# Kernel tuning notes

Measured on AMD Instinct MI355X. Metric: run time of the kernel, lower is better.

## Reference

```python
import jax, jax.numpy as jnp
import numpy as np

T, H, W = 4, 16, 16
S = T * H * W          # 1024 flattened sequence length
C = 576                # embd_dim
NH = 8                 # n_head
DK = C // NH           # 72 per-head dim
L = 4                  # n_layer
B = 4                  # batch
PD = C // 3            # 192 per-axis pos-embed dim


def setup_inputs() -> dict:
    key = jax.random.key(0)
    ks = jax.random.split(key, 10)
    s = 1.0 / np.sqrt(C)
    return {
        "x": jax.random.normal(ks[0], (B, T, H, W, C), jnp.float32),
        "pos0": jax.random.normal(ks[1], (T, PD), jnp.float32) * 0.01,
        "pos1": jax.random.normal(ks[2], (H, PD), jnp.float32) * 0.01,
        "pos2": jax.random.normal(ks[3], (W, PD), jnp.float32) * 0.01,
        "ln1_g": jnp.ones((L, C), jnp.float32),
        "ln1_b": jnp.zeros((L, C), jnp.float32),
        "wq": jax.random.normal(ks[4], (L, C, C), jnp.float32) * s,
        "wk": jax.random.normal(ks[5], (L, C, C), jnp.float32) * s,
        "wv": jax.random.normal(ks[6], (L, C, C), jnp.float32) * s,
        "wo": jax.random.normal(ks[7], (L, C, C), jnp.float32) * (s / np.sqrt(L)),
        "wo_b": jnp.zeros((L, C), jnp.float32),
        "ln2_g": jnp.ones((L, C), jnp.float32),
        "ln2_b": jnp.zeros((L, C), jnp.float32),
        "w1": jax.random.normal(ks[8], (L, C, 4 * C), jnp.float32) * s,
        "b1": jnp.zeros((L, 4 * C), jnp.float32),
        "w2": jax.random.normal(ks[9], (L, 4 * C, C), jnp.float32) * (s / 2.0),
        "b2": jnp.zeros((L, C), jnp.float32),
    }


def _layernorm(x, g, b):
    # Faithful to the source: float32 math, and (1e-5 + rsqrt(var)) multiplier
    # (note: source adds eps to rsqrt, not to var -- replicated exactly).
    xf = x.astype(jnp.float32)
    mu = xf.mean(-1, keepdims=True)
    var = jnp.mean(jnp.square(xf - mu), -1, keepdims=True)
    y = (xf - mu) * (1e-5 + jax.lax.rsqrt(var)) * g + b
    return y.astype(x.dtype)


def _stack(x, pos0, pos1, pos2, ln1_g, ln1_b, wq, wk, wv, wo, wo_b,
           ln2_g, ln2_b, w1, b1, w2, b2):
    b = x.shape[0]
    xf = x.reshape(b, S, C)
    # right_shift (decode_step=None): shift flattened tokens right by one
    xf = jnp.pad(xf[:, :-1], ((0, 0), (1, 0), (0, 0)))
    # broadcast positional embedding, concat along channel
    pos = jnp.concatenate([
        jnp.broadcast_to(pos0[:, None, None, :], (T, H, W, PD)),
        jnp.broadcast_to(pos1[None, :, None, :], (T, H, W, PD)),
        jnp.broadcast_to(pos2[None, None, :, :], (T, H, W, PD)),
    ], axis=-1).reshape(S, C)
    xf = xf + pos

    causal = jnp.tril(jnp.ones((S, S), bool))
    scale = 1.0 / np.sqrt(DK)
    neg_inf = jnp.float32(-jnp.inf)

    for l in range(L):  # fixed small layer loop
        # --- causal full self-attention ---
        h = _layernorm(xf, ln1_g[l], ln1_b[l])
        q = (h @ wq[l]).reshape(b, S, NH, DK).transpose(0, 2, 1, 3)
        k = (h @ wk[l]).reshape(b, S, NH, DK).transpose(0, 2, 1, 3)
        v = (h @ wv[l]).reshape(b, S, NH, DK).transpose(0, 2, 1, 3)
        att = jnp.einsum('bhqd,bhkd->bhqk', q, k) * scale
        att = jnp.where(causal, att, neg_inf)
        att = jax.nn.softmax(att, axis=-1)
        a = jnp.einsum('bhqk,bhkd->bhqd', att, v)
        a = a.transpose(0, 2, 1, 3).reshape(b, S, C)
        xf = xf + a @ wo[l] + wo_b[l]
        # --- FFN with GeLU2: sigmoid(1.702*x)*x ---
        h = _layernorm(xf, ln2_g[l], ln2_b[l])
        h = h @ w1[l] + b1[l]
        h = jax.nn.sigmoid(1.702 * h) * h
        xf = xf + h @ w2[l] + b2[l]
    return xf.reshape(b, T, H, W, C)


def reference(x, pos0, pos1, pos2, ln1_g, ln1_b, wq, wk, wv, wo, wo_b,
              ln2_g, ln2_b, w1, b1, w2, b2):
    return _stack(x, pos0, pos1, pos2, ln1_g, ln1_b, wq, wk, wv, wo, wo_b,
                  ln2_g, ln2_b, w1, b1, w2, b2)
```

## Files before the change

### kernel.cpp

```cpp
#include <hip/hip_runtime.h>
#include <hip/hip_bf16.h>

typedef __hip_bfloat16 bf16;
using bf16x8 = __attribute__((ext_vector_type(8))) short;
using f32x4  = __attribute__((ext_vector_type(4))) float;

#define S_LEN 1024
#define CDIM  576
#define NHEAD 8
#define DKH   72
#define BATCH 4
#define MROWS 4096
#define FFDIM 2304
#define QKVN  1728

__device__ __forceinline__ void gload16(const void* g, void* l) {
  __builtin_amdgcn_global_load_lds(
      (const __attribute__((address_space(1))) unsigned int*)g,
      (__attribute__((address_space(3))) unsigned int*)l, 16, 0, 0);
}

__device__ __forceinline__ short f2bf_bits(float x) {
  unsigned int u = __float_as_uint(x);
  u += 0x7fffu + ((u >> 16) & 1u);
  return (short)(u >> 16);
}

__global__ __launch_bounds__(256) void transpose_cvt(
    const float* __restrict__ in, bf16* __restrict__ out, int K, int N,
    size_t in_ls, size_t out_ls) {
  __shared__ float tile[32][33];
  const float* inl = in + (size_t)blockIdx.z * in_ls;
  bf16* outl = out + (size_t)blockIdx.z * out_ls;
  int n0 = blockIdx.x * 32, k0 = blockIdx.y * 32;
  int tx = threadIdx.x & 31, ty = threadIdx.x >> 5;
#pragma unroll
  for (int i = 0; i < 32; i += 8)
    tile[ty + i][tx] = inl[(size_t)(k0 + ty + i) * N + (n0 + tx)];
  __syncthreads();
#pragma unroll
  for (int i = 0; i < 32; i += 8)
    outl[(size_t)(n0 + ty + i) * K + (k0 + tx)] = __float2bfloat16(tile[tx][ty + i]);
}

__global__ __launch_bounds__(256) void build_xf(
    const float* __restrict__ x, const float* __restrict__ p0,
    const float* __restrict__ p1, const float* __restrict__ p2,
    float* __restrict__ xf) {
  int idx = blockIdx.x * 256 + threadIdx.x;
  int c4 = idx % 144;
  int s  = (idx / 144) & (S_LEN - 1);
  int b  = idx / (144 * S_LEN);
  int c  = c4 * 4;
  int t = s >> 8, hh = (s >> 4) & 15, w = s & 15;
  float4 pv;
  if (c < 192)       pv = *(const float4*)&p0[t  * 192 + c];
  else if (c < 384)  pv = *(const float4*)&p1[hh * 192 + c - 192];
  else               pv = *(const float4*)&p2[w  * 192 + c - 384];
  float4 xv = make_float4(0.f, 0.f, 0.f, 0.f);
  if (s > 0) xv = *(const float4*)&x[((size_t)b * S_LEN + s - 1) * CDIM + c];
  float4 r = make_float4(xv.x + pv.x, xv.y + pv.y, xv.z + pv.z, xv.w + pv.w);
  *(float4*)&xf[((size_t)b * S_LEN + s) * CDIM + c] = r;
}

__global__ __launch_bounds__(256) void ln_kernel(
    const float* __restrict__ x, const float* __restrict__ g,
    const float* __restrict__ b, bf16* __restrict__ out) {
  int row  = blockIdx.x * 4 + (threadIdx.x >> 6);
  int lane = threadIdx.x & 63;
  const float* xr = x + (size_t)row * CDIM;
  float vals[9];
  float sum = 0.f;
#pragma unroll
  for (int i = 0; i < 9; i++) { vals[i] = xr[lane + 64 * i]; sum += vals[i]; }
#pragma unroll
  for (int o = 1; o < 64; o <<= 1) sum += __shfl_xor(sum, o);
  float mu = sum * (1.f / CDIM);
  float vs = 0.f;
#pragma unroll
  for (int i = 0; i < 9; i++) { float d = vals[i] - mu; vs += d * d; }
#pragma unroll
  for (int o = 1; o < 64; o <<= 1) vs += __shfl_xor(vs, o);
  float mult = 1e-5f + rsqrtf(vs * (1.f / CDIM));
  bf16* orow = out + (size_t)row * CDIM;
#pragma unroll
  for (int i = 0; i < 9; i++) {
    int c = lane + 64 * i;
    orow[c] = __float2bfloat16((vals[i] - mu) * mult * g[c] + b[c]);
  }
}

template <int BM, int BN, bool BIAS, bool RES, int ACT, bool OUTBF>
__global__ __launch_bounds__(256) void gemm3(
    const bf16* __restrict__ A, const bf16* __restrict__ Bt,
    const float* __restrict__ bias, const float* __restrict__ res,
    void* __restrict__ outp, int N, int K) {
  constexpr int MI = BM / 32;
  constexpr int NI = BN / 32;
  constexpr int AJ = BM / 64;
  constexpr int BJ = BN / 64;
  __shared__ __align__(16) short ldsA[2][BM * 32];
  __shared__ __align__(16) short ldsB[2][BN * 32];
  const int tid = threadIdx.x, lane = tid & 63, wave = tid >> 6;
  const int lr = lane & 15, quad = lane >> 4;
  const int m0 = blockIdx.x * BM, n0 = blockIdx.y * BN;
  const int wm = (wave & 1) * (BM / 2), wn = (wave >> 1) * (BN / 2);
  f32x4 acc[MI][NI] = {};

  const int srow = lane >> 2, scol = (lane & 3) * 8;
  const short* Ag[AJ];
  int ldsAo[AJ];
#pragma unroll
  for (int j = 0; j < AJ; j++) {
    Ag[j] = (const short*)A + (size_t)(m0 + (wave * AJ + j) * 16 + srow) * K + scol;
    ldsAo[j] = (wave * AJ + j) * 512;
  }
  const short* Bg[BJ];
  int ldsBo[BJ];
#pragma unroll
  for (int j = 0; j < BJ; j++) {
    Bg[j] = (const short*)Bt + (size_t)(n0 + (wave * BJ + j) * 16 + srow) * K + scol;
    ldsBo[j] = (wave * BJ + j) * 512;
  }

#pragma unroll
  for (int j = 0; j < AJ; j++) gload16(Ag[j], &ldsA[0][ldsAo[j]]);
#pragma unroll
  for (int j = 0; j < BJ; j++) gload16(Bg[j], &ldsB[0][ldsBo[j]]);
  __syncthreads();

  int cur = 0;
  for (int k0 = 0; k0 < K; k0 += 32) {
    const int nxt = cur ^ 1;
    if (k0 + 32 < K) {
#pragma unroll
      for (int j = 0; j < AJ; j++) gload16(Ag[j] + k0 + 32, &ldsA[nxt][ldsAo[j]]);
#pragma unroll
      for (int j = 0; j < BJ; j++) gload16(Bg[j] + k0 + 32, &ldsB[nxt][ldsBo[j]]);
    }
    bf16x8 af[MI], bfv[NI];
#pragma unroll
    for (int mi = 0; mi < MI; mi++)
      af[mi] = *(const bf16x8*)&ldsA[cur][(wm + mi * 16 + lr) * 32 + quad * 8];
#pragma unroll
    for (int ni = 0; ni < NI; ni++)
      bfv[ni] = *(const bf16x8*)&ldsB[cur][(wn + ni * 16 + lr) * 32 + quad * 8];
#pragma unroll
    for (int mi = 0; mi < MI; mi++)
#pragma unroll
      for (int ni = 0; ni < NI; ni++)
        acc[mi][ni] = __builtin_amdgcn_mfma_f32_16x16x32_bf16(af[mi], bfv[ni], acc[mi][ni], 0, 0, 0);
    if (k0 + 32 < K) __syncthreads();
    cur = nxt;
  }

  float* fout = (float*)outp;
  bf16*  bout = (bf16*)outp;
#pragma unroll
  for (int mi = 0; mi < MI; mi++)
#pragma unroll
    for (int ni = 0; ni < NI; ni++) {
      int col = n0 + wn + ni * 16 + lr;
#pragma unroll
      for (int r = 0; r < 4; r++) {
        int row = m0 + wm + mi * 16 + quad * 4 + r;
        float v = acc[mi][ni][r];
        if (BIAS) v += bias[col];
        if (ACT == 1) v = v / (1.f + __expf(-1.702f * v));
        size_t idx = (size_t)row * N + col;
        if (RES) v += res[idx];
        if (OUTBF) bout[idx] = __float2bfloat16(v);
        else       fout[idx] = v;
      }
    }
}

__global__ __launch_bounds__(256) void attn_mfma(
    const bf16* __restrict__ qkv, bf16* __restrict__ a) {
  __shared__ __align__(16) short ldsK[2][9 * 512];
  __shared__ __align__(16) short ldsVt[2][80][104];
  __shared__ __align__(16) short ldsP[4 * 1024];
  const int bh = blockIdx.y, b = bh >> 3, h = bh & 7;
  const int tid = threadIdx.x, wave = tid >> 6, lane = tid & 63;
  const int lr = lane & 15, quad = lane >> 4;
  const int qt = 15 - (int)blockIdx.x;
  const float scale = 0.11785113019775793f;
  const int qcol = h * DKH, kcol = CDIM + h * DKH, vcol = 2 * CDIM + h * DKH;

  const int qrow = qt * 64 + wave * 16 + lr;
  const short* qg = (const short*)qkv + (size_t)(b * S_LEN + qrow) * QKVN + qcol;
  bf16x8 qfrag[3];
#pragma unroll
  for (int c = 0; c < 3; c++) {
    int d0 = c * 32 + quad * 8;
    bf16x8 z = {0, 0, 0, 0, 0, 0, 0, 0};
    qfrag[c] = (d0 < DKH) ? *(const bf16x8*)(qg + d0) : z;
  }
  f32x4 oacc[5] = {};
  float m[4], l[4];
#pragma unroll
  for (int r = 0; r < 4; r++) { m[r] = -1e30f; l[r] = 0.f; }

  const size_t ktstep = (size_t)64 * QKVN;
  const short* kg0 = (const short*)qkv + (size_t)(b * S_LEN + wave * 16 + lr) * QKVN + kcol + quad * 8;
  const short* kg2 = (const short*)qkv + (size_t)(b * S_LEN + lane) * QKVN + kcol + 64;
  const int vkey = tid & 63, vdgb = tid >> 6;
  const short* vg0 = (const short*)qkv + (size_t)(b * S_LEN + vkey) * QKVN + vcol;

  {
#pragma unroll
    for (int c = 0; c < 2; c++)
      gload16(kg0 + c * 32, &ldsK[0][(wave * 2 + c) * 512]);
    if (wave == 0) gload16(kg2, &ldsK[0][8 * 512]);
#pragma unroll
    for (int pass = 0; pass < 3; pass++) {
      int d0 = (vdgb + pass * 4) * 8;
      if (d0 < 80) {
        bf16x8 vv = {0, 0, 0, 0, 0, 0, 0, 0};
        if (d0 < DKH) vv = *(const bf16x8*)(vg0 + d0);
#pragma unroll
        for (int j = 0; j < 8; j++) ldsVt[0][d0 + j][vkey] = vv[j];
      }
    }
  }
  __syncthreads();

  for (int kt = 0; kt <= qt; kt++) {
    const int cur = kt & 1, nxt = cur ^ 1;
    const bool pf = (kt < qt);
    bf16x8 vpre[3];
    if (pf) {
      const short* kg = kg0 + (size_t)(kt + 1) * ktstep;
#pragma unroll
      for (int c = 0; c < 2; c++)
        gload16(kg + c * 32, &ldsK[nxt][(wave * 2 + c) * 512]);
      if (wave == 0) gload16(kg2 + (size_t)(kt + 1) * ktstep, &ldsK[nxt][8 * 512]);
      const short* vg = vg0 + (size_t)(kt + 1) * ktstep;
#pragma unroll
      for (int pass = 0; pass < 3; pass++) {
        int d0 = (vdgb + pass * 4) * 8;
        bf16x8 z = {0, 0, 0, 0, 0, 0, 0, 0};
        vpre[pass] = (d0 < DKH) ? *(const bf16x8*)(vg + d0) : z;
      }
    }
    f32x4 sacc[4] = {};
#pragma unroll
    for (int nc = 0; nc < 4; nc++) {
      bf16x8 kf0 = *(const bf16x8*)&ldsK[cur][(nc * 2 + 0) * 512 + lane * 8];
      sacc[nc] = __builtin_amdgcn_mfma_f32_16x16x32_bf16(qfrag[0], kf0, sacc[nc], 0, 0, 0);
      bf16x8 kf1 = *(const bf16x8*)&ldsK[cur][(nc * 2 + 1) * 512 + lane * 8];
      sacc[nc] = __builtin_amdgcn_mfma_f32_16x16x32_bf16(qfrag[1], kf1, sacc[nc], 0, 0, 0);
      bf16x8 kf2 = *(const bf16x8*)&ldsK[cur][8 * 512 + (nc * 16 + lr) * 8];
      sacc[nc] = __builtin_amdgcn_mfma_f32_16x16x32_bf16(qfrag[2], kf2, sacc[nc], 0, 0, 0);
    }
    float tmax[4];
#pragma unroll
    for (int r = 0; r < 4; r++) tmax[r] = -1e30f;
    bool diag = (kt == qt);
#pragma unroll
    for (int nc = 0; nc < 4; nc++)
#pragma unroll
      for (int r = 0; r < 4; r++) {
        float s = sacc[nc][r] * scale;
        if (diag && (nc * 16 + lr > wave * 16 + quad * 4 + r)) s = -1e30f;
        sacc[nc][r] = s;
        tmax[r] = fmaxf(tmax[r], s);
      }
#pragma unroll
    for (int r = 0; r < 4; r++) {
      tmax[r] = fmaxf(tmax[r], __shfl_xor(tmax[r], 1));
      tmax[r] = fmaxf(tmax[r], __shfl_xor(tmax[r], 2));
      tmax[r] = fmaxf(tmax[r], __shfl_xor(tmax[r], 4));
      tmax[r] = fmaxf(tmax[r], __shfl_xor(tmax[r], 8));
    }
    float alpha[4], psum[4];
#pragma unroll
    for (int r = 0; r < 4; r++) {
      float mn = fmaxf(m[r], tmax[r]);
      alpha[r] = __expf(m[r] - mn);
      m[r] = mn;
      psum[r] = 0.f;
    }
#pragma unroll
    for (int nc = 0; nc < 4; nc++)
#pragma unroll
      for (int r = 0; r < 4; r++) {
        float p = __expf(sacc[nc][r] - m[r]);
        psum[r] += p;
        int col = nc * 16 + lr;
        ldsP[wave * 1024 + (col >> 5) * 512 +
             (((col >> 3) & 3) * 16 + quad * 4 + r) * 8 + (col & 7)] = f2bf_bits(p);
      }
#pragma unroll
    for (int r = 0; r < 4; r++) {
      psum[r] += __shfl_xor(psum[r], 1);
      psum[r] += __shfl_xor(psum[r], 2);
      psum[r] += __shfl_xor(psum[r], 4);
      psum[r] += __shfl_xor(psum[r], 8);
      l[r] = l[r] * alpha[r] + psum[r];
    }
#pragma unroll
    for (int dc = 0; dc < 5; dc++)
#pragma unroll
      for (int r = 0; r < 4; r++) oacc[dc][r] *= alpha[r];
    __builtin_amdgcn_sched_barrier(0);
    bf16x8 pfrag[2];
#pragma unroll
    for (int kc = 0; kc < 2; kc++)
      pfrag[kc] = *(const bf16x8*)&ldsP[wave * 1024 + kc * 512 + lane * 8];
#pragma unroll
    for (int dc = 0; dc < 5; dc++)
#pragma unroll
      for (int kc = 0; kc < 2; kc++) {
        bf16x8 vf = *(const bf16x8*)&ldsVt[cur][dc * 16 + lr][kc * 32 + quad * 8];
        oacc[dc] = __builtin_amdgcn_mfma_f32_16x16x32_bf16(pfrag[kc], vf, oacc[dc], 0, 0, 0);
      }
    if (pf) {
#pragma unroll
      for (int pass = 0; pass < 3; pass++) {
        int d0 = (vdgb + pass * 4) * 8;
        if (d0 < 80) {
#pragma unroll
          for (int j = 0; j < 8; j++) ldsVt[nxt][d0 + j][vkey] = vpre[pass][j];
        }
      }
    }
    __syncthreads();
  }

#pragma unroll
  for (int dc = 0; dc < 5; dc++) {
    int d = dc * 16 + lr;
    if (d < DKH) {
#pragma unroll
      for (int r = 0; r < 4; r++) {
        int row = qt * 64 + wave * 16 + quad * 4 + r;
        float val = oacc[dc][r] / l[r];
        a[(size_t)(b * S_LEN + row) * CDIM + h * DKH + d] = __float2bfloat16(val);
      }
    }
  }
}

extern "C" void kernel_launch(void* const* d_in, const int* in_sizes, int n_in,
                              void* d_out, int out_size, void* d_ws, size_t ws_size,
                              hipStream_t stream) {
  const float* x    = (const float*)d_in[0];
  const float* pos0 = (const float*)d_in[1];
  const float* pos1 = (const float*)d_in[2];
  const float* pos2 = (const float*)d_in[3];
  const float* ln1g = (const float*)d_in[4];
  const float* ln1b = (const float*)d_in[5];
  const float* wq   = (const float*)d_in[6];
  const float* wk   = (const float*)d_in[7];
  const float* wv   = (const float*)d_in[8];
  const float* wo   = (const float*)d_in[9];
  const float* wob  = (const float*)d_in[10];
  const float* ln2g = (const float*)d_in[11];
  const float* ln2b = (const float*)d_in[12];
  const float* w1   = (const float*)d_in[13];
  const float* b1   = (const float*)d_in[14];
  const float* w2   = (const float*)d_in[15];
  const float* b2   = (const float*)d_in[16];

  char* ws = (char*)d_ws;
  size_t off = 0;
  auto alloc = [&](size_t bytes) {
    char* p = ws + off;
    off += (bytes + 255) & ~(size_t)255;
    return p;
  };
  bf16* wqkvT = (bf16*)alloc((size_t)4 * QKVN * CDIM * sizeof(bf16));
  bf16* woT   = (bf16*)alloc((size_t)4 * CDIM * CDIM * sizeof(bf16));
  bf16* w1T   = (bf16*)alloc((size_t)4 * FFDIM * CDIM * sizeof(bf16));
  bf16* w2T   = (bf16*)alloc((size_t)4 * CDIM * FFDIM * sizeof(bf16));
  bf16* hbuf  = (bf16*)alloc((size_t)MROWS * CDIM * sizeof(bf16));
  bf16* abuf  = (bf16*)alloc((size_t)MROWS * CDIM * sizeof(bf16));
  bf16* ubuf  = (bf16*)alloc((size_t)MROWS * FFDIM * sizeof(bf16));
  bf16* qkvb  = (bf16*)alloc((size_t)MROWS * QKVN * sizeof(bf16));
  float* xf   = (float*)d_out;

  const size_t ils  = (size_t)CDIM * CDIM;
  const size_t ils2 = (size_t)CDIM * FFDIM;
  const size_t qkv_ls = (size_t)QKVN * CDIM;
  transpose_cvt<<<dim3(18, 18, 4), 256, 0, stream>>>(wq, wqkvT, CDIM, CDIM, ils, qkv_ls);
  transpose_cvt<<<dim3(18, 18, 4), 256, 0, stream>>>(wk, wqkvT + (size_t)CDIM * CDIM, CDIM, CDIM, ils, qkv_ls);
  transpose_cvt<<<dim3(18, 18, 4), 256, 0, stream>>>(wv, wqkvT + (size_t)2 * CDIM * CDIM, CDIM, CDIM, ils, qkv_ls);
  transpose_cvt<<<dim3(18, 18, 4), 256, 0, stream>>>(wo, woT, CDIM, CDIM, ils, ils);
  transpose_cvt<<<dim3(72, 18, 4), 256, 0, stream>>>(w1, w1T, CDIM, FFDIM, ils2, ils2);
  transpose_cvt<<<dim3(18, 72, 4), 256, 0, stream>>>(w2, w2T, FFDIM, CDIM, ils2, ils2);

  build_xf<<<2304, 256, 0, stream>>>(x, pos0, pos1, pos2, xf);

  for (int l = 0; l < 4; l++) {
    bf16* wqkv_l = wqkvT + (size_t)l * qkv_ls;
    bf16* wo_l   = woT   + (size_t)l * ils;
    bf16* w1_l   = w1T   + (size_t)l * ils2;
    bf16* w2_l   = w2T   + (size_t)l * ils2;

    ln_kernel<<<1024, 256, 0, stream>>>(xf, ln1g + l * CDIM, ln1b + l * CDIM, hbuf);
    gemm3<128, 64, false, false, 0, true><<<dim3(32, QKVN / 64), 256, 0, stream>>>(
        hbuf, wqkv_l, nullptr, nullptr, qkvb, QKVN, CDIM);
    attn_mfma<<<dim3(16, 32), 256, 0, stream>>>(qkvb, abuf);
    gemm3<64, 64, true, true, 0, false><<<dim3(64, CDIM / 64), 256, 0, stream>>>(
        abuf, wo_l, wob + l * CDIM, xf, xf, CDIM, CDIM);
    ln_kernel<<<1024, 256, 0, stream>>>(xf, ln2g + l * CDIM, ln2b + l * CDIM, hbuf);
    gemm3<128, 64, true, false, 1, true><<<dim3(32, FFDIM / 64), 256, 0, stream>>>(
        hbuf, w1_l, b1 + l * FFDIM, nullptr, ubuf, FFDIM, CDIM);
    gemm3<64, 64, true, true, 0, false><<<dim3(64, CDIM / 64), 256, 0, stream>>>(
        ubuf, w2_l, b2 + l * CDIM, xf, xf, CDIM, FFDIM);
  }
}
```

Measured before the change: 779.7 us.

## Deepen GEMM LDS pipeline to four stages with prefetch distance two

```diff
diff --git a/kernel.cpp b/kernel.cpp
--- a/kernel.cpp
+++ b/kernel.cpp
@@ -18,6 +18,14 @@
   __builtin_amdgcn_global_load_lds(
       (const __attribute__((address_space(1))) unsigned int*)g,
       (__attribute__((address_space(3))) unsigned int*)l, 16, 0, 0);
+}
+
+template <int N> __device__ __forceinline__ void wait_vmcnt() {
+  if constexpr (N == 0)      asm volatile("s_waitcnt vmcnt(0)" ::: "memory");
+  else if constexpr (N == 2) asm volatile("s_waitcnt vmcnt(2)" ::: "memory");
+  else if constexpr (N == 3) asm volatile("s_waitcnt vmcnt(3)" ::: "memory");
+  else if constexpr (N == 4) asm volatile("s_waitcnt vmcnt(4)" ::: "memory");
+  else if constexpr (N == 6) asm volatile("s_waitcnt vmcnt(6)" ::: "memory");
 }
 
 __device__ __forceinline__ short f2bf_bits(float x) {
@@ -99,8 +107,9 @@
   constexpr int NI = BN / 32;
   constexpr int AJ = BM / 64;
   constexpr int BJ = BN / 64;
-  __shared__ __align__(16) short ldsA[2][BM * 32];
-  __shared__ __align__(16) short ldsB[2][BN * 32];
+  constexpr int LPS = AJ + BJ;
+  __shared__ __align__(16) short ldsA[4][BM * 32];
+  __shared__ __align__(16) short ldsB[4][BN * 32];
   const int tid = threadIdx.x, lane = tid & 63, wave = tid >> 6;
   const int lr = lane & 15, quad = lane >> 4;
   const int m0 = blockIdx.x * BM, n0 = blockIdx.y * BN;
@@ -127,31 +136,39 @@
   for (int j = 0; j < AJ; j++) gload16(Ag[j], &ldsA[0][ldsAo[j]]);
 #pragma unroll
   for (int j = 0; j < BJ; j++) gload16(Bg[j], &ldsB[0][ldsBo[j]]);
-  __syncthreads();
-
-  int cur = 0;
-  for (int k0 = 0; k0 < K; k0 += 32) {
-    const int nxt = cur ^ 1;
-    if (k0 + 32 < K) {
-#pragma unroll
-      for (int j = 0; j < AJ; j++) gload16(Ag[j] + k0 + 32, &ldsA[nxt][ldsAo[j]]);
-#pragma unroll
-      for (int j = 0; j < BJ; j++) gload16(Bg[j] + k0 + 32, &ldsB[nxt][ldsBo[j]]);
-    }
+#pragma unroll
+  for (int j = 0; j < AJ; j++) gload16(Ag[j] + 32, &ldsA[1][ldsAo[j]]);
+#pragma unroll
+  for (int j = 0; j < BJ; j++) gload16(Bg[j] + 32, &ldsB[1][ldsBo[j]]);
+
+  int bi = 0;
+  for (int k0 = 0; k0 < K; k0 += 32, bi = (bi + 1) & 3) {
+    if (k0 + 64 < K) {
+      const int sb = (bi + 2) & 3;
+#pragma unroll
+      for (int j = 0; j < AJ; j++) gload16(Ag[j] + k0 + 64, &ldsA[sb][ldsAo[j]]);
+#pragma unroll
+      for (int j = 0; j < BJ; j++) gload16(Bg[j] + k0 + 64, &ldsB[sb][ldsBo[j]]);
+      wait_vmcnt<2 * LPS>();
+    } else if (k0 + 32 < K) {
+      wait_vmcnt<LPS>();
+    } else {
+      wait_vmcnt<0>();
+    }
+    __builtin_amdgcn_s_barrier();
+    __builtin_amdgcn_sched_barrier(0);
     bf16x8 af[MI], bfv[NI];
 #pragma unroll
     for (int mi = 0; mi < MI; mi++)
-      af[mi] = *(const bf16x8*)&ldsA[cur][(wm + mi * 16 + lr) * 32 + quad * 8];
+      af[mi] = *(const bf16x8*)&ldsA[bi][(wm + mi * 16 + lr) * 32 + quad * 8];
 #pragma unroll
     for (int ni = 0; ni < NI; ni++)
-      bfv[ni] = *(const bf16x8*)&ldsB[cur][(wn + ni * 16 + lr) * 32 + quad * 8];
+      bfv[ni] = *(const bf16x8*)&ldsB[bi][(wn + ni * 16 + lr) * 32 + quad * 8];
 #pragma unroll
     for (int mi = 0; mi < MI; mi++)
 #pragma unroll
       for (int ni = 0; ni < NI; ni++)
         acc[mi][ni] = __builtin_amdgcn_mfma_f32_16x16x32_bf16(af[mi], bfv[ni], acc[mi][ni], 0, 0, 0);
-    if (k0 + 32 < K) __syncthreads();
-    cur = nxt;
   }
 
   float* fout = (float*)outp;
```

Result: faster. 719.2 us (-7.8%).
